# Optimization experiments

Hardware: AMD Instinct MI355X
Metric: run time of the kernel (lower is better)

The kernel has to match this reference:

```python
import jax, jax.numpy as jnp
import numpy as np

SPAN = 128
STRIDE = 4
LQ = 2048
LKV = 512
H = 16
DQK = 64
DV = 64
DQ = 1024
DOUT = 1024
T = SPAN // STRIDE  # table depth (rows of the sparse QK table)


def _tables():
    # Static precomputation mirroring the torch __init__ meshgrid logic.
    row, col = np.meshgrid(np.arange(T), np.arange(LQ), indexing='ij')
    qi_col = np.ceil((col - (SPAN - 1)) / STRIDE).astype(np.int64) + row  # kv index per (r, j)
    qi_row = -STRIDE * qi_col + col
    valid = (qi_row >= 0) & (qi_row < SPAN) & (qi_col >= 0) & (qi_col < LKV)
    kidx = np.clip(qi_col, 0, LKV - 1)  # clipped gather index; invalid slots masked later
    return jnp.asarray(kidx), jnp.asarray(valid)

KIDX, VALID = _tables()  # both [T, LQ]


def setup_inputs() -> dict:
    key = jax.random.key(0)
    ks = jax.random.split(key, 7)
    s = 0.02
    return {
        'q': jax.random.normal(ks[0], (2, LQ, DQ), jnp.float32),
        'k': jax.random.normal(ks[1], (2, LKV, DQ), jnp.float32),
        'v': jax.random.normal(ks[2], (2, LKV, DQ), jnp.float32),
        'Wq': jax.random.normal(ks[3], (DQ, H * DQK), jnp.float32) * s,
        'Wk': jax.random.normal(ks[4], (DQ, H * DQK), jnp.float32) * s,
        'Wv': jax.random.normal(ks[5], (DQ, H * DV), jnp.float32) * s,
        'Wo': jax.random.normal(ks[6], (H * DV, DOUT), jnp.float32) * s,
    }


def reference(q, k, v, Wq, Wk, Wv, Wo):
    B = q.shape[0]
    Q = (q @ Wq).reshape(B, LQ, H, DQK).transpose(0, 2, 1, 3)    # [B,H,LQ,DQK]
    K = (k @ Wk).reshape(B, LKV, H, DQK).transpose(0, 2, 1, 3)   # [B,H,LKV,DQK]
    V = (v @ Wv).reshape(B, LKV, H, DV).transpose(0, 2, 1, 3)    # [B,H,LKV,DV]

    # Gather K/V by the strided-span index table: [B,H,T,LQ,d]
    Kg = K[:, :, KIDX, :]
    Vg = V[:, :, KIDX, :]

    scores = jnp.einsum('bhjd,bhtjd->bhtj', Q, Kg) / np.float32(np.sqrt(DQK))
    scores = jnp.where(VALID, scores, -jnp.inf)
    probs = jax.nn.softmax(scores, axis=2)          # softmax over table rows (dim 2 in torch)
    probs = jnp.where(VALID, probs, 0.0)

    O = jnp.einsum('bhtj,bhtjd->bhjd', probs, Vg)   # [B,H,LQ,DV]
    O = O.transpose(0, 2, 1, 3).reshape(B, LQ, H * DV)
    return O @ Wo
```

## Files before the change

### kernel.cpp

```cpp
#include <hip/hip_runtime.h>
#include <hip/hip_bf16.h>

typedef __bf16 bf16x8 __attribute__((ext_vector_type(8)));
typedef float  f32x4  __attribute__((ext_vector_type(4)));
typedef unsigned short u16;
typedef unsigned int   u32;

__device__ __forceinline__ u16 f2b(float x) {
  __bf16 b = (__bf16)x;
  return __builtin_bit_cast(u16, b);
}

__device__ __forceinline__ void gload_lds16(const u16* g, u16* l) {
  __builtin_amdgcn_global_load_lds(
      (const __attribute__((address_space(1))) void*)g,
      (__attribute__((address_space(3))) void*)l, 16, 0, 0);
}

#define Q4 1048576
#define K4 262144
#define CVT_BLOCKS 6144
__global__ __launch_bounds__(256) void prep_kernel(
    const float* __restrict__ q, const float* __restrict__ k, const float* __restrict__ v,
    u16* __restrict__ qb, u16* __restrict__ kb, u16* __restrict__ vb,
    const float* __restrict__ W0, const float* __restrict__ W1,
    const float* __restrict__ W2, const float* __restrict__ W3,
    u16* __restrict__ T0, u16* __restrict__ T1, u16* __restrict__ T2, u16* __restrict__ T3)
{
  __shared__ float tile[32][33];
  int bid = blockIdx.x;
  if (bid < CVT_BLOCKS) {
    int i = bid * 256 + threadIdx.x;
    const float* src; u16* dst; int off;
    if (i < Q4)            { src = q; dst = qb; off = i; }
    else if (i < Q4 + K4)  { src = k; dst = kb; off = i - Q4; }
    else                   { src = v; dst = vb; off = i - Q4 - K4; }
    float4 x = ((const float4*)src)[off];
    ushort4 r;
    r.x = f2b(x.x); r.y = f2b(x.y); r.z = f2b(x.z); r.w = f2b(x.w);
    ((ushort4*)dst)[off] = r;
  } else {
    int t = bid - CVT_BLOCKS;
    int z = t >> 10, rem = t & 1023;
    const float* W = (z == 0) ? W0 : (z == 1) ? W1 : (z == 2) ? W2 : W3;
    u16* T = (z == 0) ? T0 : (z == 1) ? T1 : (z == 2) ? T2 : T3;
    int tx = threadIdx.x & 31, ty = threadIdx.x >> 5;
    int c0 = (rem & 31) << 5, r0 = (rem >> 5) << 5;
#pragma unroll
    for (int i = 0; i < 4; ++i)
      tile[ty + i * 8][tx] = W[(size_t)(r0 + ty + i * 8) * 1024 + c0 + tx];
    __syncthreads();
#pragma unroll
    for (int i = 0; i < 4; ++i)
      T[(size_t)(c0 + ty + i * 8) * 1024 + r0 + tx] = f2b(tile[tx][ty + i * 8]);
  }
}

template <int OUTF32>
__device__ __forceinline__ void gemm_core(
    const u16* __restrict__ A, const u16* __restrict__ Bt, void* __restrict__ C,
    int N, int K, int row0, int col0,
    u16* As0, u16* As1, u16* Bs0, u16* Bs1)
{
  const int tid = threadIdx.x;
  const int wave = tid >> 6, lane = tid & 63;
  const int wm = wave >> 1, wn = wave & 1;

  f32x4 acc[4][4] = {};

  const int srow = lane >> 3, sslot = lane & 7;
  const int scol = ((sslot ^ srow) << 3);

  const u16* gA = A + (size_t)(row0 + (wave << 5) + srow) * K + scol;
  const u16* gB = Bt + (size_t)(col0 + (wave << 5) + srow) * K + scol;

#define STAGE(as, bs, k0) do {                                           \
    _Pragma("unroll")                                                    \
    for (int i_ = 0; i_ < 4; ++i_) {                                     \
      int rb_ = (wave << 5) + (i_ << 3);                                 \
      gload_lds16(gA + (size_t)(i_ << 3) * K + (k0), (as) + (rb_ << 6)); \
      gload_lds16(gB + (size_t)(i_ << 3) * K + (k0), (bs) + (rb_ << 6)); \
    } } while (0)

  STAGE(As0, Bs0, 0);
  __syncthreads();

  u16 *asc = As0, *bsc = Bs0, *asn = As1, *bsn = Bs1;
  for (int k0 = 0; k0 < K; k0 += 64) {
    if (k0 + 64 < K) STAGE(asn, bsn, k0 + 64);
#pragma unroll
    for (int kk = 0; kk < 2; ++kk) {
      bf16x8 af[4], bfr[4];
      int colb = (kk << 6) + ((lane >> 4) << 4);
#pragma unroll
      for (int m = 0; m < 4; ++m) {
        int r = (wm << 6) + (m << 4) + (lane & 15);
        af[m] = *(const bf16x8*)((const char*)asc + (r << 7) + (colb ^ ((r & 7) << 4)));
      }
#pragma unroll
      for (int n = 0; n < 4; ++n) {
        int r = (wn << 6) + (n << 4) + (lane & 15);
        bfr[n] = *(const bf16x8*)((const char*)bsc + (r << 7) + (colb ^ ((r & 7) << 4)));
      }
#pragma unroll
      for (int m = 0; m < 4; ++m)
#pragma unroll
        for (int n = 0; n < 4; ++n)
          acc[m][n] = __builtin_amdgcn_mfma_f32_16x16x32_bf16(af[m], bfr[n], acc[m][n], 0, 0, 0);
    }
    __syncthreads();
    u16* t_;
    t_ = asc; asc = asn; asn = t_;
    t_ = bsc; bsc = bsn; bsn = t_;
  }
#undef STAGE

  const int crow = (lane >> 4) << 2;
  const int ccol = lane & 15;
#pragma unroll
  for (int m = 0; m < 4; ++m) {
#pragma unroll
    for (int n = 0; n < 4; ++n) {
      int r = row0 + (wm << 6) + (m << 4) + crow;
      int c = col0 + (wn << 6) + (n << 4) + ccol;
#pragma unroll
      for (int reg = 0; reg < 4; ++reg) {
        if (OUTF32) ((float*)C)[(size_t)(r + reg) * N + c] = acc[m][n][reg];
        else        ((u16*)C)[(size_t)(r + reg) * N + c] = f2b(acc[m][n][reg]);
      }
    }
  }
}

template <int OUTF32>
__global__ __launch_bounds__(256, 2) void gemm_bt_kernel(
    const u16* __restrict__ A, const u16* __restrict__ Bt, void* __restrict__ C,
    int M, int N, int K)
{
  __shared__ u16 As[2][8192];
  __shared__ u16 Bs[2][8192];
  const int nbx = N >> 7;
  const int bx = blockIdx.x % nbx, by = blockIdx.x / nbx;
  gemm_core<OUTF32>(A, Bt, C, N, K, by << 7, bx << 7, As[0], As[1], Bs[0], Bs[1]);
}

__global__ __launch_bounds__(256, 2) void proj_kernel(
    const u16* __restrict__ qb, const u16* __restrict__ kvb,
    const u16* __restrict__ Wqt, const u16* __restrict__ Wkt, const u16* __restrict__ Wvt,
    u16* __restrict__ Qp, u16* __restrict__ KVp)
{
  __shared__ u16 As[2][8192];
  __shared__ u16 Bs[2][8192];
  int bid = blockIdx.x;
  const u16 *A, *Bt; u16* C; int row0, col0;
  if (bid < 256) {
    A = qb; Bt = Wqt; C = Qp;
    row0 = (bid >> 3) << 7; col0 = (bid & 7) << 7;
  } else {
    int t = bid - 256;
    row0 = (t >> 3) << 7; col0 = (t & 7) << 7;
    A = kvb; C = KVp;
    Bt = (row0 >= 1024) ? Wvt : Wkt;
  }
  gemm_core<0>(A, Bt, C, 1024, 1024, row0, col0, As[0], As[1], Bs[0], Bs[1]);
}

#define VTP 56
#define PLP 72
__global__ __launch_bounds__(256) void attn_kernel(
    const u16* __restrict__ Qp, const u16* __restrict__ Kp,
    const u16* __restrict__ Vp, u16* __restrict__ Ob)
{
  __shared__ u16 Ql[64 * 64];
  __shared__ u16 Kl[48 * 64];
  __shared__ u16 Vt[64 * VTP + 64];
  __shared__ u16 Pl[64 * PLP];

  const int jt = blockIdx.x, h = blockIdx.y, b = blockIdx.z;
  const int j0 = jt << 6;
  const int kbase = (j0 - 124) >> 2;
  const int tid = threadIdx.x;
  const int wave = tid >> 6, lane = tid & 63;

  const int srow = lane >> 3, sslot = lane & 7;
  const int scol = ((sslot ^ srow) << 3);
  for (int g = wave; g < 8; g += 4) {
    int r = (g << 3) + srow;
    const u16* ga = Qp + (((size_t)(b * 2048 + j0 + r)) << 10) + (h << 6) + scol;
    gload_lds16(ga, &Ql[g << 9]);
  }
  for (int g = wave; g < 6; g += 4) {
    int r = (g << 3) + srow;
    int key = kbase + r;
    key = key < 0 ? 0 : (key > 511 ? 511 : key);
    const u16* gk = Kp + (((size_t)(b * 512 + key)) << 10) + (h << 6) + scol;
    gload_lds16(gk, &Kl[g << 9]);
  }
  for (int idx = tid; idx < 48 * 8; idx += 256) {
    int row = idx >> 3, seg = idx & 7;
    int key = kbase + row;
    key = key < 0 ? 0 : (key > 511 ? 511 : key);
    uint4 x = *(const uint4*)(Vp + (((size_t)(b * 512 + key)) << 10) + (h << 6) + (seg << 3));
    int d0 = seg << 3;
    Vt[(d0 + 0) * VTP + row] = (u16)(x.x);
    Vt[(d0 + 1) * VTP + row] = (u16)(x.x >> 16);
    Vt[(d0 + 2) * VTP + row] = (u16)(x.y);
    Vt[(d0 + 3) * VTP + row] = (u16)(x.y >> 16);
    Vt[(d0 + 4) * VTP + row] = (u16)(x.z);
    Vt[(d0 + 5) * VTP + row] = (u16)(x.z >> 16);
    Vt[(d0 + 6) * VTP + row] = (u16)(x.w);
    Vt[(d0 + 7) * VTP + row] = (u16)(x.w >> 16);
  }
  if (tid < 64) *(uint4*)&Vt[tid * VTP + 48] = make_uint4(0, 0, 0, 0);
  else if (tid < 72) *(uint4*)&Vt[64 * VTP + ((tid - 64) << 3)] = make_uint4(0, 0, 0, 0);
  __syncthreads();

  f32x4 sacc[3] = {};
  const int frow_a = (wave << 4) + (lane & 15);
#pragma unroll
  for (int kk = 0; kk < 2; ++kk) {
    int colb = (kk << 6) + ((lane >> 4) << 4);
    bf16x8 aq = *(const bf16x8*)((const char*)Ql + (frow_a << 7) + (colb ^ ((frow_a & 7) << 4)));
#pragma unroll
    for (int nt = 0; nt < 3; ++nt) {
      int rk = (nt << 4) + (lane & 15);
      bf16x8 bk = *(const bf16x8*)((const char*)Kl + (rk << 7) + (colb ^ ((rk & 7) << 4)));
      sacc[nt] = __builtin_amdgcn_mfma_f32_16x16x32_bf16(aq, bk, sacc[nt], 0, 0, 0);
    }
  }

  const int rof = (wave << 2) + (lane >> 4);
  const int cb0 = lane & 15;
  bool vld[3]; float sc[3][4];
#pragma unroll
  for (int nt = 0; nt < 3; ++nt) {
    int c = cb0 + (nt << 4);
    vld[nt] = ((unsigned)(c - rof) < 32u) && (kbase + c >= 0);
#pragma unroll
    for (int r = 0; r < 4; ++r) sc[nt][r] = sacc[nt][r] * 0.125f;
  }
  float mx[4], rs[4];
#pragma unroll
  for (int r = 0; r < 4; ++r) {
    float m = -3.0e38f;
#pragma unroll
    for (int nt = 0; nt < 3; ++nt) m = vld[nt] ? fmaxf(m, sc[nt][r]) : m;
    m = fmaxf(m, __shfl_xor(m, 1));
    m = fmaxf(m, __shfl_xor(m, 2));
    m = fmaxf(m, __shfl_xor(m, 4));
    m = fmaxf(m, __shfl_xor(m, 8));
    mx[r] = m;
  }
#pragma unroll
  for (int r = 0; r < 4; ++r) {
    float s = 0.f;
#pragma unroll
    for (int nt = 0; nt < 3; ++nt) {
      float e = vld[nt] ? __expf(sc[nt][r] - mx[r]) : 0.f;
      sc[nt][r] = e;
      s += e;
    }
    s += __shfl_xor(s, 1);
    s += __shfl_xor(s, 2);
    s += __shfl_xor(s, 4);
    s += __shfl_xor(s, 8);
    rs[r] = 1.f / s;
  }
#pragma unroll
  for (int r = 0; r < 4; ++r) {
    int jq = (wave << 4) + ((lane >> 4) << 2) + r;
#pragma unroll
    for (int nt = 0; nt < 3; ++nt)
      Pl[jq * PLP + cb0 + (nt << 4)] = f2b(sc[nt][r] * rs[r]);
    Pl[jq * PLP + 48 + cb0] = 0;
  }
  __syncthreads();

  f32x4 oacc[4] = {};
#pragma unroll
  for (int kk = 0; kk < 2; ++kk) {
    int koff = (kk << 5) + ((lane >> 4) << 3);
    bf16x8 ap = *(const bf16x8*)&Pl[frow_a * PLP + koff];
#pragma unroll
    for (int nt = 0; nt < 4; ++nt) {
      int dr = (nt << 4) + (lane & 15);
      bf16x8 bv = *(const bf16x8*)&Vt[dr * VTP + koff];
      oacc[nt] = __builtin_amdgcn_mfma_f32_16x16x32_bf16(ap, bv, oacc[nt], 0, 0, 0);
    }
  }

#pragma unroll
  for (int nt = 0; nt < 4; ++nt) {
    int d = (nt << 4) + (lane & 15);
#pragma unroll
    for (int r = 0; r < 4; ++r) {
      int jq = (wave << 4) + ((lane >> 4) << 2) + r;
      Ob[(((size_t)(b * 2048 + j0 + jq)) << 10) + (h << 6) + d] = f2b(oacc[nt][r]);
    }
  }
}

extern "C" void kernel_launch(void* const* d_in, const int* in_sizes, int n_in,
                              void* d_out, int out_size, void* d_ws, size_t ws_size,
                              hipStream_t stream) {
  const float* q  = (const float*)d_in[0];
  const float* k  = (const float*)d_in[1];
  const float* v  = (const float*)d_in[2];
  const float* Wq = (const float*)d_in[3];
  const float* Wk = (const float*)d_in[4];
  const float* Wv = (const float*)d_in[5];
  const float* Wo = (const float*)d_in[6];

  char* ws = (char*)d_ws;
  const size_t MB = 1u << 20;
  u16* qb  = (u16*)(ws + 0 * MB);
  u16* kb  = (u16*)(ws + 8 * MB);
  u16* vb  = (u16*)(ws + 10 * MB);
  u16* Wqt = (u16*)(ws + 12 * MB);
  u16* Wkt = (u16*)(ws + 14 * MB);
  u16* Wvt = (u16*)(ws + 16 * MB);
  u16* Wot = (u16*)(ws + 18 * MB);
  u16* Qp  = (u16*)(ws + 20 * MB);
  u16* Kp  = (u16*)(ws + 28 * MB);
  u16* Vp  = (u16*)(ws + 30 * MB);
  u16* Ob  = (u16*)(ws + 32 * MB);

  prep_kernel<<<CVT_BLOCKS + 4096, 256, 0, stream>>>(
      q, k, v, qb, kb, vb, Wq, Wk, Wv, Wo, Wqt, Wkt, Wvt, Wot);
  proj_kernel<<<384, 256, 0, stream>>>(qb, kb, Wqt, Wkt, Wvt, Qp, Kp);
  attn_kernel<<<dim3(32, 16, 2), 256, 0, stream>>>(Qp, Kp, Vp, Ob);
  gemm_bt_kernel<1><<<256, 256, 0, stream>>>(Ob, Wot, d_out, 4096, 1024, 1024);
}
```

Before: 60.79 us.

## Fuse all four stages into one persistent kernel with grid barriers

Replaces the four launches (prep, projection, attention, output GEMM) with a single persistent kernel of 256 blocks. The blocks synchronise between stages through atomic-counter grid barriers and share one LDS union across stages. The attention output now reuses the qb buffer. This removes launch gaps and the tail of each kernel, but it runs fewer blocks per stage (384 projection tiles and 1024 attention tiles are looped over 256 blocks), assumes all 256 blocks are co-resident, and adds barrier spin cost.

```diff
diff --git a/kernel.cpp b/kernel.cpp
--- a/kernel.cpp
+++ b/kernel.cpp
@@ -6,6 +6,8 @@
 typedef unsigned short u16;
 typedef unsigned int   u32;
 
+#define NBLK 256
+
 __device__ __forceinline__ u16 f2b(float x) {
   __bf16 b = (__bf16)x;
   return __builtin_bit_cast(u16, b);
@@ -17,47 +19,26 @@
       (__attribute__((address_space(3))) void*)l, 16, 0, 0);
 }
 
-#define Q4 1048576
-#define K4 262144
-#define CVT_BLOCKS 6144
-__global__ __launch_bounds__(256) void prep_kernel(
-    const float* __restrict__ q, const float* __restrict__ k, const float* __restrict__ v,
-    u16* __restrict__ qb, u16* __restrict__ kb, u16* __restrict__ vb,
-    const float* __restrict__ W0, const float* __restrict__ W1,
-    const float* __restrict__ W2, const float* __restrict__ W3,
-    u16* __restrict__ T0, u16* __restrict__ T1, u16* __restrict__ T2, u16* __restrict__ T3)
-{
-  __shared__ float tile[32][33];
-  int bid = blockIdx.x;
-  if (bid < CVT_BLOCKS) {
-    int i = bid * 256 + threadIdx.x;
-    const float* src; u16* dst; int off;
-    if (i < Q4)            { src = q; dst = qb; off = i; }
-    else if (i < Q4 + K4)  { src = k; dst = kb; off = i - Q4; }
-    else                   { src = v; dst = vb; off = i - Q4 - K4; }
-    float4 x = ((const float4*)src)[off];
-    ushort4 r;
-    r.x = f2b(x.x); r.y = f2b(x.y); r.z = f2b(x.z); r.w = f2b(x.w);
-    ((ushort4*)dst)[off] = r;
-  } else {
-    int t = bid - CVT_BLOCKS;
-    int z = t >> 10, rem = t & 1023;
-    const float* W = (z == 0) ? W0 : (z == 1) ? W1 : (z == 2) ? W2 : W3;
-    u16* T = (z == 0) ? T0 : (z == 1) ? T1 : (z == 2) ? T2 : T3;
-    int tx = threadIdx.x & 31, ty = threadIdx.x >> 5;
-    int c0 = (rem & 31) << 5, r0 = (rem >> 5) << 5;
-#pragma unroll
-    for (int i = 0; i < 4; ++i)
-      tile[ty + i * 8][tx] = W[(size_t)(r0 + ty + i * 8) * 1024 + c0 + tx];
-    __syncthreads();
-#pragma unroll
-    for (int i = 0; i < 4; ++i)
-      T[(size_t)(c0 + ty + i * 8) * 1024 + r0 + tx] = f2b(tile[tx][ty + i * 8]);
-  }
+__device__ __forceinline__ void grid_barrier(u32* cnt, int idx) {
+  __threadfence();
+  __syncthreads();
+  if (threadIdx.x == 0) {
+    atomicAdd(&cnt[idx * 16], 1u);
+    while (__hip_atomic_load(&cnt[idx * 16], __ATOMIC_RELAXED,
+                             __HIP_MEMORY_SCOPE_AGENT) < NBLK) {
+      __builtin_amdgcn_s_sleep(1);
+    }
+  }
+  __syncthreads();
+  __threadfence();
+}
+
+__global__ void zero_cnt_kernel(u32* cnt) {
+  if (threadIdx.x < 64) cnt[threadIdx.x] = 0;
 }
 
 template <int OUTF32>
-__device__ __forceinline__ void gemm_core(
+__device__ __forceinline__ void gemm_tile(
     const u16* __restrict__ A, const u16* __restrict__ Bt, void* __restrict__ C,
     int N, int K, int row0, int col0,
     u16* As0, u16* As1, u16* Bs0, u16* Bs1)
@@ -132,51 +113,13 @@
   }
 }
 
-template <int OUTF32>
-__global__ __launch_bounds__(256, 2) void gemm_bt_kernel(
-    const u16* __restrict__ A, const u16* __restrict__ Bt, void* __restrict__ C,
-    int M, int N, int K)
-{
-  __shared__ u16 As[2][8192];
-  __shared__ u16 Bs[2][8192];
-  const int nbx = N >> 7;
-  const int bx = blockIdx.x % nbx, by = blockIdx.x / nbx;
-  gemm_core<OUTF32>(A, Bt, C, N, K, by << 7, bx << 7, As[0], As[1], Bs[0], Bs[1]);
-}
-
-__global__ __launch_bounds__(256, 2) void proj_kernel(
-    const u16* __restrict__ qb, const u16* __restrict__ kvb,
-    const u16* __restrict__ Wqt, const u16* __restrict__ Wkt, const u16* __restrict__ Wvt,
-    u16* __restrict__ Qp, u16* __restrict__ KVp)
-{
-  __shared__ u16 As[2][8192];
-  __shared__ u16 Bs[2][8192];
-  int bid = blockIdx.x;
-  const u16 *A, *Bt; u16* C; int row0, col0;
-  if (bid < 256) {
-    A = qb; Bt = Wqt; C = Qp;
-    row0 = (bid >> 3) << 7; col0 = (bid & 7) << 7;
-  } else {
-    int t = bid - 256;
-    row0 = (t >> 3) << 7; col0 = (t & 7) << 7;
-    A = kvb; C = KVp;
-    Bt = (row0 >= 1024) ? Wvt : Wkt;
-  }
-  gemm_core<0>(A, Bt, C, 1024, 1024, row0, col0, As[0], As[1], Bs[0], Bs[1]);
-}
-
 #define VTP 56
 #define PLP 72
-__global__ __launch_bounds__(256) void attn_kernel(
+__device__ __forceinline__ void attn_tile(
     const u16* __restrict__ Qp, const u16* __restrict__ Kp,
-    const u16* __restrict__ Vp, u16* __restrict__ Ob)
+    const u16* __restrict__ Vp, u16* __restrict__ Ob,
+    int jt, int h, int b, u16* Ql, u16* Kl, u16* Vt, u16* Pl)
 {
-  __shared__ u16 Ql[64 * 64];
-  __shared__ u16 Kl[48 * 64];
-  __shared__ u16 Vt[64 * VTP + 64];
-  __shared__ u16 Pl[64 * PLP];
-
-  const int jt = blockIdx.x, h = blockIdx.y, b = blockIdx.z;
   const int j0 = jt << 6;
   const int kbase = (j0 - 124) >> 2;
   const int tid = threadIdx.x;
@@ -300,18 +243,22 @@
   }
 }
 
-extern "C" void kernel_launch(void* const* d_in, const int* in_sizes, int n_in,
-                              void* d_out, int out_size, void* d_ws, size_t ws_size,
-                              hipStream_t stream) {
-  const float* q  = (const float*)d_in[0];
-  const float* k  = (const float*)d_in[1];
-  const float* v  = (const float*)d_in[2];
-  const float* Wq = (const float*)d_in[3];
-  const float* Wk = (const float*)d_in[4];
-  const float* Wv = (const float*)d_in[5];
-  const float* Wo = (const float*)d_in[6];
-
-  char* ws = (char*)d_ws;
+#define Q4 1048576
+#define K4 262144
+
+union SharedU {
+  struct { u16 As[2][8192]; u16 Bs[2][8192]; } g;
+  struct { u16 Ql[4096]; u16 Kl[3072]; u16 Vt[64 * VTP + 64]; u16 Pl[64 * PLP]; } a;
+  float tp[32][33];
+};
+
+__global__ __launch_bounds__(256) void fused_kernel(
+    const float* __restrict__ q, const float* __restrict__ k, const float* __restrict__ v,
+    const float* __restrict__ W0, const float* __restrict__ W1,
+    const float* __restrict__ W2, const float* __restrict__ W3,
+    float* __restrict__ out, char* __restrict__ ws)
+{
+  __shared__ SharedU sh;
   const size_t MB = 1u << 20;
   u16* qb  = (u16*)(ws + 0 * MB);
   u16* kb  = (u16*)(ws + 8 * MB);
@@ -323,11 +270,103 @@
   u16* Qp  = (u16*)(ws + 20 * MB);
   u16* Kp  = (u16*)(ws + 28 * MB);
   u16* Vp  = (u16*)(ws + 30 * MB);
-  u16* Ob  = (u16*)(ws + 32 * MB);
-
-  prep_kernel<<<CVT_BLOCKS + 4096, 256, 0, stream>>>(
-      q, k, v, qb, kb, vb, Wq, Wk, Wv, Wo, Wqt, Wkt, Wvt, Wot);
-  proj_kernel<<<384, 256, 0, stream>>>(qb, kb, Wqt, Wkt, Wvt, Qp, Kp);
-  attn_kernel<<<dim3(32, 16, 2), 256, 0, stream>>>(Qp, Kp, Vp, Ob);
-  gemm_bt_kernel<1><<<256, 256, 0, stream>>>(Ob, Wot, d_out, 4096, 1024, 1024);
-}
+  u16* Ob  = qb;
+  u32* cnt = (u32*)(ws + 32 * MB);
+
+  const int bid = blockIdx.x;
+  const int tid = threadIdx.x;
+  const int gtid = bid * 256 + tid;
+  const int NT = NBLK * 256;
+
+  {
+    const float4* s4 = (const float4*)q;
+    ushort4* d4 = (ushort4*)qb;
+    for (int base = gtid; base < Q4; base += NT * 4) {
+      float4 x0 = s4[base], x1 = s4[base + NT], x2 = s4[base + 2 * NT], x3 = s4[base + 3 * NT];
+      ushort4 r0, r1, r2, r3;
+      r0.x = f2b(x0.x); r0.y = f2b(x0.y); r0.z = f2b(x0.z); r0.w = f2b(x0.w);
+      r1.x = f2b(x1.x); r1.y = f2b(x1.y); r1.z = f2b(x1.z); r1.w = f2b(x1.w);
+      r2.x = f2b(x2.x); r2.y = f2b(x2.y); r2.z = f2b(x2.z); r2.w = f2b(x2.w);
+      r3.x = f2b(x3.x); r3.y = f2b(x3.y); r3.z = f2b(x3.z); r3.w = f2b(x3.w);
+      d4[base] = r0; d4[base + NT] = r1; d4[base + 2 * NT] = r2; d4[base + 3 * NT] = r3;
+    }
+    const float4* sk = (const float4*)k;
+    const float4* sv = (const float4*)v;
+    ushort4* dk = (ushort4*)kb;
+    ushort4* dv = (ushort4*)vb;
+    for (int base = gtid; base < K4; base += NT * 2) {
+      float4 x0 = sk[base], x1 = sk[base + NT], x2 = sv[base], x3 = sv[base + NT];
+      ushort4 r0, r1, r2, r3;
+      r0.x = f2b(x0.x); r0.y = f2b(x0.y); r0.z = f2b(x0.z); r0.w = f2b(x0.w);
+      r1.x = f2b(x1.x); r1.y = f2b(x1.y); r1.z = f2b(x1.z); r1.w = f2b(x1.w);
+      r2.x = f2b(x2.x); r2.y = f2b(x2.y); r2.z = f2b(x2.z); r2.w = f2b(x2.w);
+      r3.x = f2b(x3.x); r3.y = f2b(x3.y); r3.z = f2b(x3.z); r3.w = f2b(x3.w);
+      dk[base] = r0; dk[base + NT] = r1; dv[base] = r2; dv[base + NT] = r3;
+    }
+    int tx = tid & 31, ty = tid >> 5;
+    for (int tt = bid; tt < 4096; tt += NBLK) {
+      int z = tt >> 10, rem = tt & 1023;
+      const float* W = (z == 0) ? W0 : (z == 1) ? W1 : (z == 2) ? W2 : W3;
+      u16* T = (z == 0) ? Wqt : (z == 1) ? Wkt : (z == 2) ? Wvt : Wot;
+      int c0 = (rem & 31) << 5, r0 = (rem >> 5) << 5;
+      __syncthreads();
+#pragma unroll
+      for (int i = 0; i < 4; ++i)
+        sh.tp[ty + i * 8][tx] = W[(size_t)(r0 + ty + i * 8) * 1024 + c0 + tx];
+      __syncthreads();
+#pragma unroll
+      for (int i = 0; i < 4; ++i)
+        T[(size_t)(c0 + ty + i * 8) * 1024 + r0 + tx] = f2b(sh.tp[tx][ty + i * 8]);
+    }
+  }
+  grid_barrier(cnt, 0);
+
+  for (int t = bid; t < 384; t += NBLK) {
+    __syncthreads();
+    const u16 *A, *Bt; u16* C; int row0, col0;
+    if (t < 256) {
+      A = qb; Bt = Wqt; C = Qp;
+      row0 = (t >> 3) << 7; col0 = (t & 7) << 7;
+    } else {
+      int t2 = t - 256;
+      row0 = (t2 >> 3) << 7; col0 = (t2 & 7) << 7;
+      A = kb; C = Kp;
+      Bt = (row0 >= 1024) ? Wvt : Wkt;
+    }
+    gemm_tile<0>(A, Bt, C, 1024, 1024, row0, col0,
+                 sh.g.As[0], sh.g.As[1], sh.g.Bs[0], sh.g.Bs[1]);
+  }
+  grid_barrier(cnt, 1);
+
+  for (int t = bid; t < 1024; t += NBLK) {
+    __syncthreads();
+    int jt = t & 31, h = (t >> 5) & 15, b = t >> 9;
+    attn_tile(Qp, Kp, Vp, Ob, jt, h, b, sh.a.Ql, sh.a.Kl, sh.a.Vt, sh.a.Pl);
+  }
+  grid_barrier(cnt, 2);
+
+  {
+    int t = bid;
+    int row0 = (t >> 3) << 7, col0 = (t & 7) << 7;
+    gemm_tile<1>(Ob, Wot, out, 1024, 1024, row0, col0,
+                 sh.g.As[0], sh.g.As[1], sh.g.Bs[0], sh.g.Bs[1]);
+  }
+}
+
+extern "C" void kernel_launch(void* const* d_in, const int* in_sizes, int n_in,
+                              void* d_out, int out_size, void* d_ws, size_t ws_size,
+                              hipStream_t stream) {
+  const float* q  = (const float*)d_in[0];
+  const float* k  = (const float*)d_in[1];
+  const float* v  = (const float*)d_in[2];
+  const float* Wq = (const float*)d_in[3];
+  const float* Wk = (const float*)d_in[4];
+  const float* Wv = (const float*)d_in[5];
+  const float* Wo = (const float*)d_in[6];
+
+  char* ws = (char*)d_ws;
+  u32* cnt = (u32*)(ws + (size_t)(32u << 20));
+
+  zero_cnt_kernel<<<1, 64, 0, stream>>>(cnt);
+  fused_kernel<<<NBLK, 256, 0, stream>>>(q, k, v, Wq, Wk, Wv, Wo, (float*)d_out, ws);
+}
```

Result: slower. 231.2 us (+280.4%).

## Fuse fp32-to-bf16 activation conversion into projection GEMM A-tile loads

Applied to the files above, without the earlier changes.

The projection GEMM now reads fp32 q/k/v straight from global memory into registers, converts them to bf16 and stores them into LDS, so the separate conversion pass and its bf16 workspace round trip are gone. The prep kernel now only transposes and casts the weights. Both GEMM kernels also remap block indices so consecutive blocks are spread across row tiles, which is meant to improve L2 reuse of the weight columns. In exchange, the A loads go through registers instead of direct global-to-LDS loads, and each K step adds an extra barrier, which may reduce overlap between loads and MFMA work.

```diff
diff --git a/kernel.cpp b/kernel.cpp
--- a/kernel.cpp
+++ b/kernel.cpp
@@ -17,42 +17,85 @@
       (__attribute__((address_space(3))) void*)l, 16, 0, 0);
 }
 
-#define Q4 1048576
-#define K4 262144
-#define CVT_BLOCKS 6144
+__device__ __forceinline__ void cvt8_store(u16* dst, float4 a, float4 b) {
+  union { u16 u[8]; uint4 v; } r;
+  r.u[0] = f2b(a.x); r.u[1] = f2b(a.y); r.u[2] = f2b(a.z); r.u[3] = f2b(a.w);
+  r.u[4] = f2b(b.x); r.u[5] = f2b(b.y); r.u[6] = f2b(b.z); r.u[7] = f2b(b.w);
+  *(uint4*)dst = r.v;
+}
+
 __global__ __launch_bounds__(256) void prep_kernel(
-    const float* __restrict__ q, const float* __restrict__ k, const float* __restrict__ v,
-    u16* __restrict__ qb, u16* __restrict__ kb, u16* __restrict__ vb,
     const float* __restrict__ W0, const float* __restrict__ W1,
     const float* __restrict__ W2, const float* __restrict__ W3,
     u16* __restrict__ T0, u16* __restrict__ T1, u16* __restrict__ T2, u16* __restrict__ T3)
 {
   __shared__ float tile[32][33];
-  int bid = blockIdx.x;
-  if (bid < CVT_BLOCKS) {
-    int i = bid * 256 + threadIdx.x;
-    const float* src; u16* dst; int off;
-    if (i < Q4)            { src = q; dst = qb; off = i; }
-    else if (i < Q4 + K4)  { src = k; dst = kb; off = i - Q4; }
-    else                   { src = v; dst = vb; off = i - Q4 - K4; }
-    float4 x = ((const float4*)src)[off];
-    ushort4 r;
-    r.x = f2b(x.x); r.y = f2b(x.y); r.z = f2b(x.z); r.w = f2b(x.w);
-    ((ushort4*)dst)[off] = r;
-  } else {
-    int t = bid - CVT_BLOCKS;
-    int z = t >> 10, rem = t & 1023;
-    const float* W = (z == 0) ? W0 : (z == 1) ? W1 : (z == 2) ? W2 : W3;
-    u16* T = (z == 0) ? T0 : (z == 1) ? T1 : (z == 2) ? T2 : T3;
-    int tx = threadIdx.x & 31, ty = threadIdx.x >> 5;
-    int c0 = (rem & 31) << 5, r0 = (rem >> 5) << 5;
-#pragma unroll
-    for (int i = 0; i < 4; ++i)
-      tile[ty + i * 8][tx] = W[(size_t)(r0 + ty + i * 8) * 1024 + c0 + tx];
-    __syncthreads();
-#pragma unroll
-    for (int i = 0; i < 4; ++i)
-      T[(size_t)(c0 + ty + i * 8) * 1024 + r0 + tx] = f2b(tile[tx][ty + i * 8]);
+  int t = blockIdx.x;
+  int z = t >> 10, rem = t & 1023;
+  const float* W = (z == 0) ? W0 : (z == 1) ? W1 : (z == 2) ? W2 : W3;
+  u16* T = (z == 0) ? T0 : (z == 1) ? T1 : (z == 2) ? T2 : T3;
+  int tx = threadIdx.x & 31, ty = threadIdx.x >> 5;
+  int c0 = (rem & 31) << 5, r0 = (rem >> 5) << 5;
+#pragma unroll
+  for (int i = 0; i < 4; ++i)
+    tile[ty + i * 8][tx] = W[(size_t)(r0 + ty + i * 8) * 1024 + c0 + tx];
+  __syncthreads();
+#pragma unroll
+  for (int i = 0; i < 4; ++i)
+    T[(size_t)(c0 + ty + i * 8) * 1024 + r0 + tx] = f2b(tile[tx][ty + i * 8]);
+}
+
+__device__ __forceinline__ void compute_step(
+    const u16* asc, const u16* bsc, int lane, int wm, int wn, f32x4 (&acc)[4][4])
+{
+#pragma unroll
+  for (int kk = 0; kk < 2; ++kk) {
+    bf16x8 af[4], bfr[4];
+    int colb = (kk << 6) + ((lane >> 4) << 4);
+#pragma unroll
+    for (int m = 0; m < 4; ++m) {
+      int r = (wm << 6) + (m << 4) + (lane & 15);
+      af[m] = *(const bf16x8*)((const char*)asc + (r << 7) + (colb ^ ((r & 7) << 4)));
+    }
+#pragma unroll
+    for (int n = 0; n < 4; ++n) {
+      int r = (wn << 6) + (n << 4) + (lane & 15);
+      bfr[n] = *(const bf16x8*)((const char*)bsc + (r << 7) + (colb ^ ((r & 7) << 4)));
+    }
+#pragma unroll
+    for (int m = 0; m < 4; ++m)
+#pragma unroll
+      for (int n = 0; n < 4; ++n)
+        acc[m][n] = __builtin_amdgcn_mfma_f32_16x16x32_bf16(af[m], bfr[n], acc[m][n], 0, 0, 0);
+  }
+}
+
+__device__ __forceinline__ void stage_b(const u16* gB, u16* bs, int wave, int K, int k0) {
+#pragma unroll
+  for (int i = 0; i < 4; ++i) {
+    int rb = (wave << 5) + (i << 3);
+    gload_lds16(gB + (size_t)(i << 3) * K + k0, bs + (rb << 6));
+  }
+}
+
+template <int OUTF32>
+__device__ __forceinline__ void cwrite(
+    void* C, int N, int row0, int col0, int lane, int wm, int wn, f32x4 (&acc)[4][4])
+{
+  const int crow = (lane >> 4) << 2;
+  const int ccol = lane & 15;
+#pragma unroll
+  for (int m = 0; m < 4; ++m) {
+#pragma unroll
+    for (int n = 0; n < 4; ++n) {
+      int r = row0 + (wm << 6) + (m << 4) + crow;
+      int c = col0 + (wn << 6) + (n << 4) + ccol;
+#pragma unroll
+      for (int reg = 0; reg < 4; ++reg) {
+        if (OUTF32) ((float*)C)[(size_t)(r + reg) * N + c] = acc[m][n][reg];
+        else        ((u16*)C)[(size_t)(r + reg) * N + c] = f2b(acc[m][n][reg]);
+      }
+    }
   }
 }
 
@@ -65,71 +108,85 @@
   const int tid = threadIdx.x;
   const int wave = tid >> 6, lane = tid & 63;
   const int wm = wave >> 1, wn = wave & 1;
-
   f32x4 acc[4][4] = {};
 
   const int srow = lane >> 3, sslot = lane & 7;
   const int scol = ((sslot ^ srow) << 3);
-
   const u16* gA = A + (size_t)(row0 + (wave << 5) + srow) * K + scol;
   const u16* gB = Bt + (size_t)(col0 + (wave << 5) + srow) * K + scol;
 
-#define STAGE(as, bs, k0) do {                                           \
-    _Pragma("unroll")                                                    \
-    for (int i_ = 0; i_ < 4; ++i_) {                                     \
-      int rb_ = (wave << 5) + (i_ << 3);                                 \
-      gload_lds16(gA + (size_t)(i_ << 3) * K + (k0), (as) + (rb_ << 6)); \
-      gload_lds16(gB + (size_t)(i_ << 3) * K + (k0), (bs) + (rb_ << 6)); \
-    } } while (0)
-
-  STAGE(As0, Bs0, 0);
+  stage_b(gA, As0, wave, K, 0);
+  stage_b(gB, Bs0, wave, K, 0);
   __syncthreads();
 
   u16 *asc = As0, *bsc = Bs0, *asn = As1, *bsn = Bs1;
   for (int k0 = 0; k0 < K; k0 += 64) {
-    if (k0 + 64 < K) STAGE(asn, bsn, k0 + 64);
-#pragma unroll
-    for (int kk = 0; kk < 2; ++kk) {
-      bf16x8 af[4], bfr[4];
-      int colb = (kk << 6) + ((lane >> 4) << 4);
-#pragma unroll
-      for (int m = 0; m < 4; ++m) {
-        int r = (wm << 6) + (m << 4) + (lane & 15);
-        af[m] = *(const bf16x8*)((const char*)asc + (r << 7) + (colb ^ ((r & 7) << 4)));
-      }
-#pragma unroll
-      for (int n = 0; n < 4; ++n) {
-        int r = (wn << 6) + (n << 4) + (lane & 15);
-        bfr[n] = *(const bf16x8*)((const char*)bsc + (r << 7) + (colb ^ ((r & 7) << 4)));
-      }
-#pragma unroll
-      for (int m = 0; m < 4; ++m)
-#pragma unroll
-        for (int n = 0; n < 4; ++n)
-          acc[m][n] = __builtin_amdgcn_mfma_f32_16x16x32_bf16(af[m], bfr[n], acc[m][n], 0, 0, 0);
-    }
+    if (k0 + 64 < K) {
+      stage_b(gA, asn, wave, K, k0 + 64);
+      stage_b(gB, bsn, wave, K, k0 + 64);
+    }
+    compute_step(asc, bsc, lane, wm, wn, acc);
     __syncthreads();
     u16* t_;
     t_ = asc; asc = asn; asn = t_;
     t_ = bsc; bsc = bsn; bsn = t_;
   }
-#undef STAGE
-
-  const int crow = (lane >> 4) << 2;
-  const int ccol = lane & 15;
-#pragma unroll
-  for (int m = 0; m < 4; ++m) {
-#pragma unroll
-    for (int n = 0; n < 4; ++n) {
-      int r = row0 + (wm << 6) + (m << 4) + crow;
-      int c = col0 + (wn << 6) + (n << 4) + ccol;
-#pragma unroll
-      for (int reg = 0; reg < 4; ++reg) {
-        if (OUTF32) ((float*)C)[(size_t)(r + reg) * N + c] = acc[m][n][reg];
-        else        ((u16*)C)[(size_t)(r + reg) * N + c] = f2b(acc[m][n][reg]);
+  cwrite<OUTF32>(C, N, row0, col0, lane, wm, wn, acc);
+}
+
+__device__ __forceinline__ void gemm_core_f32a(
+    const float* __restrict__ Af,
+    const u16* __restrict__ Bt, u16* __restrict__ C,
+    int N, int K, int row0, int col0,
+    u16* As0, u16* As1, u16* Bs0, u16* Bs1)
+{
+  const int tid = threadIdx.x;
+  const int wave = tid >> 6, lane = tid & 63;
+  const int wm = wave >> 1, wn = wave & 1;
+  f32x4 acc[4][4] = {};
+
+  const int srow = lane >> 3, sslot = lane & 7;
+  const int scol = ((sslot ^ srow) << 3);
+  const float* gAf = Af + (size_t)((wave << 5) + srow) * K + scol;
+  const u16*  gB  = Bt + (size_t)(col0 + (wave << 5) + srow) * K + scol;
+  const int awbase = (lane << 3);
+
+  float4 a0[4], a1[4];
+#pragma unroll
+  for (int i = 0; i < 4; ++i) {
+    const float* g = gAf + (size_t)(i << 3) * K;
+    a0[i] = *(const float4*)g; a1[i] = *(const float4*)(g + 4);
+  }
+  stage_b(gB, Bs0, wave, K, 0);
+#pragma unroll
+  for (int i = 0; i < 4; ++i)
+    cvt8_store(As0 + (((wave << 5) + (i << 3)) << 6) + awbase, a0[i], a1[i]);
+  __syncthreads();
+
+  u16 *asc = As0, *bsc = Bs0, *asn = As1, *bsn = Bs1;
+  for (int k0 = 0; k0 < K; k0 += 64) {
+    const bool more = (k0 + 64) < K;
+    if (more) {
+#pragma unroll
+      for (int i = 0; i < 4; ++i) {
+        const float* g = gAf + (size_t)(i << 3) * K + (k0 + 64);
+        a0[i] = *(const float4*)g; a1[i] = *(const float4*)(g + 4);
       }
-    }
-  }
+      stage_b(gB, bsn, wave, K, k0 + 64);
+    }
+    compute_step(asc, bsc, lane, wm, wn, acc);
+    __syncthreads();
+    if (more) {
+#pragma unroll
+      for (int i = 0; i < 4; ++i)
+        cvt8_store(asn + (((wave << 5) + (i << 3)) << 6) + awbase, a0[i], a1[i]);
+    }
+    __syncthreads();
+    u16* t_;
+    t_ = asc; asc = asn; asn = t_;
+    t_ = bsc; bsc = bsn; bsn = t_;
+  }
+  cwrite<0>(C, N, row0, col0, lane, wm, wn, acc);
 }
 
 template <int OUTF32>
@@ -139,30 +196,33 @@
 {
   __shared__ u16 As[2][8192];
   __shared__ u16 Bs[2][8192];
-  const int nbx = N >> 7;
-  const int bx = blockIdx.x % nbx, by = blockIdx.x / nbx;
+  int bid = blockIdx.x;
+  int t = (bid & 7) * 32 + (bid >> 3);
+  const int bx = t & 7, by = t >> 3;
   gemm_core<OUTF32>(A, Bt, C, N, K, by << 7, bx << 7, As[0], As[1], Bs[0], Bs[1]);
 }
 
 __global__ __launch_bounds__(256, 2) void proj_kernel(
-    const u16* __restrict__ qb, const u16* __restrict__ kvb,
+    const float* __restrict__ q, const float* __restrict__ k, const float* __restrict__ v,
     const u16* __restrict__ Wqt, const u16* __restrict__ Wkt, const u16* __restrict__ Wvt,
     u16* __restrict__ Qp, u16* __restrict__ KVp)
 {
   __shared__ u16 As[2][8192];
   __shared__ u16 Bs[2][8192];
   int bid = blockIdx.x;
-  const u16 *A, *Bt; u16* C; int row0, col0;
-  if (bid < 256) {
-    A = qb; Bt = Wqt; C = Qp;
-    row0 = (bid >> 3) << 7; col0 = (bid & 7) << 7;
+  int t = (bid & 7) * 48 + (bid >> 3);
+  const float* Af; const u16* Bt; u16* C; int row0, col0;
+  if (t < 256) {
+    row0 = (t >> 3) << 7; col0 = (t & 7) << 7;
+    Af = q + (size_t)row0 * 1024; Bt = Wqt; C = Qp;
   } else {
-    int t = bid - 256;
-    row0 = (t >> 3) << 7; col0 = (t & 7) << 7;
-    A = kvb; C = KVp;
-    Bt = (row0 >= 1024) ? Wvt : Wkt;
-  }
-  gemm_core<0>(A, Bt, C, 1024, 1024, row0, col0, As[0], As[1], Bs[0], Bs[1]);
+    int t2 = t - 256;
+    row0 = (t2 >> 3) << 7; col0 = (t2 & 7) << 7;
+    if (row0 < 1024) { Af = k + (size_t)row0 * 1024; Bt = Wkt; }
+    else             { Af = v + (size_t)(row0 - 1024) * 1024; Bt = Wvt; }
+    C = KVp;
+  }
+  gemm_core_f32a(Af, Bt, C, 1024, 1024, row0, col0, As[0], As[1], Bs[0], Bs[1]);
 }
 
 #define VTP 56
@@ -313,21 +373,17 @@
 
   char* ws = (char*)d_ws;
   const size_t MB = 1u << 20;
-  u16* qb  = (u16*)(ws + 0 * MB);
-  u16* kb  = (u16*)(ws + 8 * MB);
-  u16* vb  = (u16*)(ws + 10 * MB);
-  u16* Wqt = (u16*)(ws + 12 * MB);
-  u16* Wkt = (u16*)(ws + 14 * MB);
-  u16* Wvt = (u16*)(ws + 16 * MB);
-  u16* Wot = (u16*)(ws + 18 * MB);
-  u16* Qp  = (u16*)(ws + 20 * MB);
-  u16* Kp  = (u16*)(ws + 28 * MB);
-  u16* Vp  = (u16*)(ws + 30 * MB);
-  u16* Ob  = (u16*)(ws + 32 * MB);
-
-  prep_kernel<<<CVT_BLOCKS + 4096, 256, 0, stream>>>(
-      q, k, v, qb, kb, vb, Wq, Wk, Wv, Wo, Wqt, Wkt, Wvt, Wot);
-  proj_kernel<<<384, 256, 0, stream>>>(qb, kb, Wqt, Wkt, Wvt, Qp, Kp);
+  u16* Wqt = (u16*)(ws + 0 * MB);
+  u16* Wkt = (u16*)(ws + 2 * MB);
+  u16* Wvt = (u16*)(ws + 4 * MB);
+  u16* Wot = (u16*)(ws + 6 * MB);
+  u16* Qp  = (u16*)(ws + 8 * MB);
+  u16* Kp  = (u16*)(ws + 16 * MB);
+  u16* Vp  = (u16*)(ws + 18 * MB);
+  u16* Ob  = (u16*)(ws + 20 * MB);
+
+  prep_kernel<<<4096, 256, 0, stream>>>(Wq, Wk, Wv, Wo, Wqt, Wkt, Wvt, Wot);
+  proj_kernel<<<384, 256, 0, stream>>>(q, k, v, Wqt, Wkt, Wvt, Qp, Kp);
   attn_kernel<<<dim3(32, 16, 2), 256, 0, stream>>>(Qp, Kp, Vp, Ob);
   gemm_bt_kernel<1><<<256, 256, 0, stream>>>(Ob, Wot, d_out, 4096, 1024, 1024);
 }
```

After: 59.63 us. About the same (-1.9%).
